# Kernel tuning notes

Hardware: AMD Instinct MI355X
Metric: run time of the kernel (lower is better)

## Reference

```python
import jax, jax.numpy as jnp
import numpy as np
from jax import lax

NUM_CLS = 80
N_INST = 100  # instances per image (static stand-in for NMS-selected boxes)
PARAM_DIM = 169  # (8+2)*8 + 8*8 + 8 + 8 + 8 + 1
MIC = 8  # mask_inner_channels


def conv2d(x, w, b=None, padding='SAME'):
    y = lax.conv_general_dilated(x, w, (1, 1), padding,
                                 dimension_numbers=('NCHW', 'OIHW', 'NCHW'))
    if b is not None:
        y = y + b[None, :, None, None]
    return y


def group_norm(x, g, b, groups, eps=1e-5):
    N, C, H, W = x.shape
    xr = x.reshape(N, groups, C // groups, H, W)
    mu = xr.mean(axis=(2, 3, 4), keepdims=True)
    var = xr.var(axis=(2, 3, 4), keepdims=True)
    xr = (xr - mu) * lax.rsqrt(var + eps)
    return xr.reshape(N, C, H, W) * g[None, :, None, None] + b[None, :, None, None]


def resize_bilinear_ac(x, oh, ow):
    # bilinear, align_corners=True (matches F.interpolate(..., align_corners=True))
    N, C, H, W = x.shape
    ys = jnp.linspace(0.0, H - 1.0, oh)
    xs = jnp.linspace(0.0, W - 1.0, ow)
    y0 = jnp.floor(ys).astype(jnp.int32); y1 = jnp.minimum(y0 + 1, H - 1); wy = (ys - y0).astype(x.dtype)
    x0 = jnp.floor(xs).astype(jnp.int32); x1 = jnp.minimum(x0 + 1, W - 1); wx = (xs - x0).astype(x.dtype)
    top = x[:, :, y0, :] * (1.0 - wy)[None, None, :, None] + x[:, :, y1, :] * wy[None, None, :, None]
    out = top[:, :, :, x0] * (1.0 - wx)[None, None, None, :] + top[:, :, :, x1] * wx[None, None, None, :]
    return out


def head_branch(f, head_w, head_gn_g, head_gn_b, head_out_w, head_out_b, scale):
    x = f
    for i in range(4):  # bones: conv3x3 (no bias) + GN(32) + ReLU
        x = jax.nn.relu(group_norm(conv2d(x, head_w[i]), head_gn_g[i], head_gn_b[i], 32))
    x = x * scale
    return conv2d(x, head_out_w, head_out_b)


def mask_branch(feats, ref_w, ref_gn_g, ref_gn_b, tow_w, tow_gn_g, tow_gn_b, out_w, out_gn_g, out_gn_b):
    x = None
    th, tw = feats[0].shape[2:]
    for i, f in enumerate(feats):
        xp = jax.nn.relu(group_norm(conv2d(f, ref_w[i]), ref_gn_g[i], ref_gn_b[i], 1))
        if i == 0:
            x = xp
        else:
            x = x + resize_bilinear_ac(xp, th, tw)
    for i in range(4):
        x = jax.nn.relu(group_norm(conv2d(x, tow_w[i]), tow_gn_g[i], tow_gn_b[i], 1))
    x = jax.nn.relu(group_norm(conv2d(x, out_w), out_gn_g, out_gn_b, 1))
    return x


def dynamic_conv(mask_feats, params):
    # mask_feats: [B, 8, h, w]; params: [B*N, 169] per-instance generated weights/biases
    B, C, h, w = mask_feats.shape
    n = params.shape[0]
    w1 = params[:, :80].reshape(n, MIC, C + 2)        # 1x1 conv 10->8
    w2 = params[:, 80:144].reshape(n, MIC, MIC)       # 1x1 conv 8->8
    w3 = params[:, 144:152].reshape(n, 1, MIC)        # 1x1 conv 8->1
    b1 = params[:, 152:160]
    b2 = params[:, 160:168]
    b3 = params[:, 168:169]
    # gather per-instance feature maps (img_ids = repeat of image index)
    x = jnp.repeat(mask_feats, n // B, axis=0)        # [n, 8, h, w]
    xr = jnp.linspace(-1.0, 1.0, w, dtype=mask_feats.dtype)
    yr = jnp.linspace(-1.0, 1.0, h, dtype=mask_feats.dtype)
    yy, xx = jnp.meshgrid(yr, xr, indexing='ij')
    coords = jnp.broadcast_to(jnp.stack([xx, yy], axis=0)[None], (n, 2, h, w))
    x = jnp.concatenate([x, coords], axis=1)          # [n, 10, h, w]
    x = jax.nn.relu(jnp.einsum('noc,nchw->nohw', w1, x) + b1[:, :, None, None])
    x = jax.nn.relu(jnp.einsum('noc,nchw->nohw', w2, x) + b2[:, :, None, None])
    x = jnp.einsum('noc,nchw->nohw', w3, x) + b3[:, :, None, None]
    return resize_bilinear_ac(x, 2 * h, 2 * w)        # [n, 1, 2h, 2w]


def condinst_forward(f3, f4, f5, f6, f7, head_w, head_gn_g, head_gn_b, head_out_w,
                     head_out_b, scales, ref_w, ref_gn_g, ref_gn_b, tow_w, tow_gn_g,
                     tow_gn_b, out_w, out_gn_g, out_gn_b):
    feats = [f3, f4, f5, f6, f7]
    preds = [head_branch(f, head_w, head_gn_g, head_gn_b, head_out_w, head_out_b, scales[i])
             for i, f in enumerate(feats)]
    mask_feats = mask_branch(feats[:3], ref_w, ref_gn_g, ref_gn_b,
                             tow_w, tow_gn_g, tow_gn_b, out_w, out_gn_g, out_gn_b)
    # controller params: take first N_INST P3 locations (static stand-in for NMS top-k)
    B = f3.shape[0]
    ctrl = preds[0][:, NUM_CLS + 5:, :, :].reshape(B, PARAM_DIM, -1)  # [B, 169, HW]
    params = jnp.transpose(ctrl[:, :, :N_INST], (0, 2, 1)).reshape(B * N_INST, PARAM_DIM)
    mask_logits = dynamic_conv(mask_feats, params)
    return (*preds, mask_feats, mask_logits)


def setup_inputs() -> dict:
    key = jax.random.key(0)
    ks = jax.random.split(key, 12)
    B = 2
    inp = {
        'f3': jax.random.normal(ks[0], (B, 256, 96, 160), jnp.float32),
        'f4': jax.random.normal(ks[1], (B, 256, 48, 80), jnp.float32),
        'f5': jax.random.normal(ks[2], (B, 256, 24, 40), jnp.float32),
        'f6': jax.random.normal(ks[3], (B, 256, 12, 20), jnp.float32),
        'f7': jax.random.normal(ks[4], (B, 256, 6, 10), jnp.float32),
        'head_w': 0.01 * jax.random.normal(ks[5], (4, 256, 256, 3, 3), jnp.float32),
        'head_gn_g': jnp.ones((4, 256), jnp.float32),
        'head_gn_b': jnp.zeros((4, 256), jnp.float32),
        'head_out_w': 0.01 * jax.random.normal(ks[6], (254, 256, 3, 3), jnp.float32),
        'head_out_b': jnp.zeros((254,), jnp.float32).at[:NUM_CLS].set(-np.log((1 - 0.01) / 0.01)),
        'scales': jnp.ones((5,), jnp.float32),
        'ref_w': 0.01 * jax.random.normal(ks[7], (3, 128, 256, 3, 3), jnp.float32),
        'ref_gn_g': jnp.ones((3, 128), jnp.float32),
        'ref_gn_b': jnp.zeros((3, 128), jnp.float32),
        'tow_w': 0.01 * jax.random.normal(ks[8], (4, 128, 128, 3, 3), jnp.float32),
        'tow_gn_g': jnp.ones((4, 128), jnp.float32),
        'tow_gn_b': jnp.zeros((4, 128), jnp.float32),
        'out_w': 0.01 * jax.random.normal(ks[9], (8, 128, 1, 1), jnp.float32),
        'out_gn_g': jnp.ones((8,), jnp.float32),
        'out_gn_b': jnp.zeros((8,), jnp.float32),
    }
    return inp


def reference(f3, f4, f5, f6, f7, head_w, head_gn_g, head_gn_b, head_out_w, head_out_b,
              scales, ref_w, ref_gn_g, ref_gn_b, tow_w, tow_gn_g, tow_gn_b, out_w,
              out_gn_g, out_gn_b):
    return condinst_forward(f3, f4, f5, f6, f7, head_w, head_gn_g, head_gn_b,
                            head_out_w, head_out_b, scales, ref_w, ref_gn_g, ref_gn_b,
                            tow_w, tow_gn_g, tow_gn_b, out_w, out_gn_g, out_gn_b)
```

## Files before the change

kernel.cpp:

```cpp
#include <hip/hip_runtime.h>
#include <hip/hip_bf16.h>

typedef __hip_bfloat16 bf16;
typedef short v8s __attribute__((ext_vector_type(8)));
typedef float v4f __attribute__((ext_vector_type(4)));

__device__ __forceinline__ float cvt(bf16 v) { return __bfloat162float(v); }

__device__ __forceinline__ float ldg_any(const void* p, size_t i, bool bf) {
    return bf ? cvt(((const bf16*)p)[i]) : ((const float*)p)[i];
}
__device__ __forceinline__ void stg_any(void* p, size_t i, float v, bool bf) {
    if (bf) ((bf16*)p)[i] = __float2bfloat16(v);
    else    ((float*)p)[i] = v;
}
__device__ __forceinline__ bool bfmode(int mode, const int* flags) {
    return mode == 2 ? (flags[0] != 0) : (mode != 0);
}
__device__ __forceinline__ unsigned short f2b(float f) {
    bf16 h = __float2bfloat16(f); return *(unsigned short*)&h;
}
__device__ __forceinline__ void b2f2(unsigned u, float& a, float& b) {
    a = __uint_as_float(u << 16);
    b = __uint_as_float(u & 0xffff0000u);
}

union U16x8 { uint4 u; unsigned short s[8]; };

#define BARLDS() asm volatile("s_waitcnt lgkmcnt(0)\n\ts_barrier" ::: "memory")

__global__ void detect_k(const unsigned int* __restrict__ x, int* __restrict__ flags)
{
    unsigned int u = x[threadIdx.x];
    int e = (u >> 23) & 0xFF;
    unsigned long long m = __ballot(e >= 200);
    if (threadIdx.x == 0) flags[0] = (m != 0ULL) ? 1 : 0;
}

__global__ void repack_off_k(const void* __restrict__ w, size_t w_off,
                             const int* __restrict__ flags, bf16* __restrict__ dst,
                             int Cout, int Cpad, int Cin, int total)
{
    const bool fw = flags[0] != 0;
    int i = blockIdx.x * 256 + threadIdx.x;
    if (i >= total) return;
    int ci = i % Cin; int r = i / Cin; int co = r % Cpad; int tap = r / Cpad;
    float v = 0.f;
    if (co < Cout) v = ldg_any(w, w_off + ((size_t)co * Cin + ci) * 9 + tap, fw);
    dst[i] = __float2bfloat16(v);
}

__global__ void padT_k(const void* __restrict__ src, const int* __restrict__ flags,
                       bf16* __restrict__ dst, int C, int H, int W, int Wq, int Hp,
                       int PIX, long total)
{
    const bool fb = flags[0] != 0;
    long v = (long)blockIdx.x * 256 + threadIdx.x;
    if (v >= total) return;
    const int C8 = C >> 3;
    int oct = (int)(v & (C8 - 1));
    long rest = v >> (C == 256 ? 5 : 4);
    int px = (int)(rest % Wq);
    long r2 = rest / Wq;
    int py = (int)(r2 % Hp);
    int n  = (int)(r2 / Hp);
    U16x8 o;
    if (py == 0 || py > H || px == 0 || px > W) {
        o.u = uint4{0, 0, 0, 0};
    } else {
        const int HW = H * W;
        size_t sb = ((size_t)n * C + oct * 8) * HW + (size_t)(py - 1) * W + (px - 1);
#pragma unroll
        for (int e = 0; e < 8; ++e) o.s[e] = f2b(ldg_any(src, sb + (size_t)e * HW, fb));
    }
    *(uint4*)(dst + v * 8) = o.u;
}

__global__ __launch_bounds__(256, 2) void conv3x3_mfma_k(
    const bf16* __restrict__ in,
    const bf16* __restrict__ wrep,
    const float* __restrict__ gstat, const void* __restrict__ gamma,
    const void* __restrict__ beta, size_t gb_off, int cpg, int Gn, float inv_pg,
    const void* __restrict__ bias, const void* __restrict__ scale, int sidx,
    void* __restrict__ out, int outm, size_t out_off, int out_C,
    const int* __restrict__ flags,
    int Cin, int H, int W, int Wq, int PIX, int Cout, int Cpad, int co_blocks)
{
    const bool fw   = flags[0] != 0;
    const bool fout = bfmode(outm, flags);

    const int t    = threadIdx.x;
    const int lane = t & 63;
    const int wv   = t >> 6;
    const int c    = lane & 15;
    const int quad = lane >> 4;
    const int wr   = wv >> 1;
    const int wc   = wv & 1;
    const int x0   = blockIdx.x * 32;
    const int y0   = blockIdx.y * 4;
    const int n    = blockIdx.z / co_blocks;
    const int cb   = blockIdx.z % co_blocks;

    __shared__ __align__(16) char s_arena[77312];
    float* s_scale = (float*)(s_arena + 75264);
    float* s_shift = (float*)(s_arena + 76288);

    const bool donorm = (gstat != nullptr);

    v4f acc[4][4];
#pragma unroll
    for (int i = 0; i < 4; ++i)
#pragma unroll
        for (int j = 0; j < 4; ++j) acc[i][j] = v4f{0.f, 0.f, 0.f, 0.f};

    const bf16* inb = in + (size_t)n * PIX * Cin;

    int goff[4], loff[4], okm[4], octv[4];
#pragma unroll
    for (int it = 0; it < 4; ++it) {
        int flat = t + 256 * it;
        int pos = flat >> 2, oct = flat & 3;
        int r = (pos * 241) >> 13;
        int cc = pos - r * 34;
        int py = y0 + r, px = x0 + cc;
        bool valid = flat < 816;
        goff[it] = (py * Wq + px) * Cin + oct * 8;
        loff[it] = valid ? (pos * 64 + (((oct + (pos >> 1)) & 3) << 4)) : -1;
        okm[it]  = (py >= 1 && py <= H && px >= 1 && px <= W) ? 1 : 0;
        octv[it] = oct * 8;
    }

    uint4 L[4];
    uint4 wrg[6];

#define STAGE_LOAD(ci0_) { \
    _Pragma("unroll") for (int it = 0; it < 4; ++it) \
        if (loff[it] >= 0) L[it] = *(const uint4*)(inb + goff[it] + (ci0_)); }

#define STAGE_WRITE(ci0_, b_) { \
    char* db = s_arena + (b_) * 13056; \
    _Pragma("unroll") for (int it = 0; it < 4; ++it) { \
        if (loff[it] < 0) continue; \
        uint4 q = L[it]; \
        if (donorm) { \
            U16x8 u_; u_.u = q; U16x8 o_; \
            if (okm[it]) { \
                int cib = (ci0_) + octv[it]; \
                _Pragma("unroll") for (int e = 0; e < 8; ++e) { \
                    float v_ = __uint_as_float((unsigned)u_.s[e] << 16); \
                    v_ = fmaxf(fmaf(v_, s_scale[cib + e], s_shift[cib + e]), 0.f); \
                    o_.s[e] = f2b(v_); } \
            } else { o_.u = uint4{0, 0, 0, 0}; } \
            q = o_.u; } \
        *(uint4*)(db + loff[it]) = q; } }

#define WLOAD(ci0_, g_) { \
    _Pragma("unroll") for (int j = 0; j < 6; ++j) { \
        int f_ = t + 256 * j; int tapl_ = f_ >> 9; int rem_ = f_ & 511; \
        wrg[j] = *(const uint4*)(wrep + ((size_t)(3 * (g_) + tapl_) * Cpad \
                 + cb * 128 + (rem_ >> 2)) * (size_t)Cin + (ci0_) + (rem_ & 3) * 8); } }

#define WSTORE(b_) { \
    bf16* sw = (bf16*)(s_arena + 26112 + (b_) * 24576); \
    _Pragma("unroll") for (int j = 0; j < 6; ++j) { \
        int f_ = t + 256 * j; int tapl_ = f_ >> 9; int rem_ = f_ & 511; \
        int co_ = rem_ >> 2; int oc_ = (rem_ + co_ + (co_ >> 2)) & 3; \
        *(uint4*)(&sw[tapl_ * 4096 + co_ * 32 + oc_ * 8]) = wrg[j]; } }

#define MPHASE(ib_, wb_, g_) { \
    const char* sb_ = s_arena + (ib_) * 13056; \
    const bf16* wp_ = (const bf16*)(s_arena + 26112 + (wb_) * 24576); \
    _Pragma("unroll") for (int kx = 0; kx < 3; ++kx) { \
        v8s bfr[4]; \
        _Pragma("unroll") for (int nf = 0; nf < 4; ++nf) { \
            int pos = (2 * wr + (nf >> 1) + (g_)) * 34 + kx + c + (nf & 1) * 16; \
            bfr[nf] = *(const v8s*)(sb_ + pos * 64 + (((quad + (pos >> 1)) & 3) << 4)); } \
        _Pragma("unroll") for (int mf = 0; mf < 4; ++mf) { \
            int col_ = wc * 64 + mf * 16 + c; \
            int os_ = (quad + col_ + (col_ >> 2)) & 3; \
            v8s af = *(const v8s*)(wp_ + kx * 4096 + col_ * 32 + os_ * 8); \
            _Pragma("unroll") for (int nf = 0; nf < 4; ++nf) \
                acc[mf][nf] = __builtin_amdgcn_mfma_f32_16x16x32_bf16( \
                    af, bfr[nf], acc[mf][nf], 0, 0, 0); } } }

    STAGE_LOAD(0);
    WLOAD(0, 0);
    if (donorm) {
        for (int ch = t; ch < Cin; ch += 256) {
            int gl = n * Gn + ch / cpg;
            float mu  = gstat[2 * gl] * inv_pg;
            float var = fmaxf(gstat[2 * gl + 1] * inv_pg - mu * mu, 0.f);
            float iv  = rsqrtf(var + 1e-5f);
            float ga  = ldg_any(gamma, gb_off + ch, fw);
            float be  = ldg_any(beta,  gb_off + ch, fw);
            s_scale[ch] = iv * ga;
            s_shift[ch] = be - mu * iv * ga;
        }
    }
    BARLDS();
    STAGE_WRITE(0, 0);
    WSTORE(0);
    BARLDS();

    for (int ci0 = 0; ci0 < Cin; ci0 += 64) {
        const bool moreB = (ci0 + 64 < Cin);
        STAGE_LOAD(ci0 + 32);
        WLOAD(ci0, 1);
        MPHASE(0, 0, 0);
        WSTORE(1);
        BARLDS();
        WLOAD(ci0, 2);
        MPHASE(0, 1, 1);
        WSTORE(0);
        BARLDS();
        WLOAD(ci0 + 32, 0);
        MPHASE(0, 0, 2);
        STAGE_WRITE(ci0 + 32, 1);
        WSTORE(1);
        BARLDS();
        if (moreB) STAGE_LOAD(ci0 + 64);
        WLOAD(ci0 + 32, 1);
        MPHASE(1, 1, 0);
        WSTORE(0);
        BARLDS();
        WLOAD(ci0 + 32, 2);
        MPHASE(1, 0, 1);
        WSTORE(1);
        BARLDS();
        if (moreB) { WLOAD(ci0 + 64, 0); }
        MPHASE(1, 1, 2);
        if (moreB) { STAGE_WRITE(ci0 + 64, 0); WSTORE(0); }
        BARLDS();
    }
#undef MPHASE
#undef WSTORE
#undef WLOAD
#undef STAGE_WRITE
#undef STAGE_LOAD

    if (outm == 0) {
        char* tb = s_arena;
#pragma unroll
        for (int mf = 0; mf < 4; ++mf) {
            int s0 = wc * 8 + mf * 2 + (quad >> 1);
#pragma unroll
            for (int nf = 0; nf < 4; ++nf) {
                int lp = (2 * wr + (nf >> 1)) * 32 + (nf & 1) * 16 + c;
                uint2 o;
                o.x = f2b(acc[mf][nf][0]) | ((unsigned)f2b(acc[mf][nf][1]) << 16);
                o.y = f2b(acc[mf][nf][2]) | ((unsigned)f2b(acc[mf][nf][3]) << 16);
                *(uint2*)(tb + lp * 256 + ((s0 ^ (lp & 7)) << 4) + (quad & 1) * 8) = o;
            }
        }
        BARLDS();
        bf16* ob = (bf16*)out + (size_t)n * PIX * out_C + cb * 128;
        const int o8 = t & 15;
#pragma unroll
        for (int pass = 0; pass < 8; ++pass) {
            int lp = pass * 16 + (t >> 4);
            uint4 q = *(const uint4*)(tb + lp * 256 + ((o8 ^ (lp & 7)) << 4));
            int y = y0 + (lp >> 5);
            int x = x0 + (lp & 31);
            if (y < H && x < W)
                *(uint4*)(ob + ((size_t)(y + 1) * Wq + (x + 1)) * out_C + o8 * 8) = q;
        }
    } else {
        const float al = scale ? ldg_any(scale, sidx, fw) : 1.f;
        const int HW = H * W;
        const int ybase = y0 + 2 * wr;
#pragma unroll
        for (int mf = 0; mf < 4; ++mf) {
            int cobase = cb * 128 + wc * 64 + mf * 16 + quad * 4;
#pragma unroll
            for (int reg = 0; reg < 4; ++reg) {
                int co = cobase + reg;
                if (co >= Cout) continue;
                float bv = bias ? ldg_any(bias, co, fw) : 0.f;
                size_t obase = out_off + ((size_t)n * Cout + co) * HW;
#pragma unroll
                for (int nf = 0; nf < 4; ++nf) {
                    int y = ybase + (nf >> 1);
                    int x = x0 + (nf & 1) * 16 + c;
                    if (y < H && x < W)
                        stg_any(out, obase + (size_t)y * W + x,
                                fmaf(al, acc[mf][nf][reg], bv), fout);
                }
            }
        }
    }
}

__global__ __launch_bounds__(256) void gn_stats_nhwc(const bf16* __restrict__ x,
                                                     float* __restrict__ stats,
                                                     int C8, int cpg8, int Gn,
                                                     long nvec, int planeC)
{
    const int n = blockIdx.z;
    const bf16* xp = x + (size_t)n * planeC;
    const int t = threadIdx.x;
    const int oct = t & (C8 - 1);
    float s = 0.f, ss = 0.f;
    const long stride = 256L * gridDim.x;
    for (long v = (long)blockIdx.x * 256 + t; v < nvec; v += stride) {
        uint4 u = *(const uint4*)(xp + v * 8);
        float f0,f1,f2,f3,f4,f5,f6,f7;
        b2f2(u.x, f0, f1); b2f2(u.y, f2, f3); b2f2(u.z, f4, f5); b2f2(u.w, f6, f7);
        s += ((f0+f1)+(f2+f3)) + ((f4+f5)+(f6+f7));
        ss = fmaf(f0,f0,ss); ss = fmaf(f1,f1,ss); ss = fmaf(f2,f2,ss); ss = fmaf(f3,f3,ss);
        ss = fmaf(f4,f4,ss); ss = fmaf(f5,f5,ss); ss = fmaf(f6,f6,ss); ss = fmaf(f7,f7,ss);
    }
    for (int off = C8; off < 64; off <<= 1) {
        s  += __shfl_xor(s,  off, 64);
        ss += __shfl_xor(ss, off, 64);
    }
    __shared__ float red[4][32][2];
    const int wvi = t >> 6;
    if ((t & 63) < C8) { red[wvi][oct][0] = s; red[wvi][oct][1] = ss; }
    __syncthreads();
    if (t < C8) {
        s  = red[0][t][0] + red[1][t][0] + red[2][t][0] + red[3][t][0];
        ss = red[0][t][1] + red[1][t][1] + red[2][t][1] + red[3][t][1];
        for (int off = cpg8 >> 1; off >= 1; off >>= 1) {
            s  += __shfl_down(s,  off, 64);
            ss += __shfl_down(ss, off, 64);
        }
        if ((t & (cpg8 - 1)) == 0) {
            int gl = n * Gn + t / cpg8;
            atomicAdd(&stats[2 * gl],     s);
            atomicAdd(&stats[2 * gl + 1], ss);
        }
    }
}

__global__ void gn_apply_nhwc(bf16* __restrict__ x, const float* __restrict__ stats,
                              const void* __restrict__ gamma, const void* __restrict__ beta,
                              size_t gb_off, const int* __restrict__ flags,
                              int C, int cpg, int Gn, int H, int W, int Wq, int PIX,
                              float inv_len, long total)
{
    const bool fw = flags[0] != 0;
    long v = (long)blockIdx.x * 256 + threadIdx.x;
    if (v >= total) return;
    const int C8 = C >> 3;
    int oct = (int)(v & (C8 - 1));
    long rest = v / C8;
    int x2 = (int)(rest % W);
    long r2 = rest / W;
    int y = (int)(r2 % H);
    int n = (int)(r2 / H);
    int ch0 = oct * 8;
    int gl = n * Gn + ch0 / cpg;
    float mu  = stats[2 * gl] * inv_len;
    float var = fmaxf(stats[2 * gl + 1] * inv_len - mu * mu, 0.f);
    float iv  = rsqrtf(var + 1e-5f);
    size_t base = ((size_t)n * PIX + (size_t)(y + 1) * Wq + (x2 + 1)) * C + ch0;
    U16x8 u; u.u = *(const uint4*)(x + base);
    U16x8 o;
#pragma unroll
    for (int e = 0; e < 8; ++e) {
        float ga = ldg_any(gamma, gb_off + ch0 + e, fw);
        float be = ldg_any(beta,  gb_off + ch0 + e, fw);
        float f = __uint_as_float((unsigned)u.s[e] << 16);
        f = fmaxf(fmaf(f, iv * ga, be - mu * iv * ga), 0.f);
        o.s[e] = f2b(f);
    }
    *(uint4*)(x + base) = o.u;
}

__global__ void extract_params_k(const void* __restrict__ pred3, const int* __restrict__ flags,
                                 float* __restrict__ prm, int HW)
{
    const bool bf = flags[0] != 0;
    int tid = blockIdx.x * blockDim.x + threadIdx.x;
    if (tid >= 200 * 169) return;
    int p = tid / 169, c = tid - p * 169;
    int b = p / 100, i = p - b * 100;
    prm[tid] = ldg_any(pred3, ((size_t)b * 254 + 85 + c) * HW + i, bf);
}

__global__ void upsample_add_nhwc(const bf16* __restrict__ src, bf16* __restrict__ dst,
                                  int h, int w, int sWq, int sPIX,
                                  int OH, int OW, int dWq, int dPIX, long total)
{
    long i = (long)blockIdx.x * 256 + threadIdx.x;
    if (i >= total) return;
    const int C = 128, C8 = 16;
    int oct = (int)(i & (C8 - 1));
    long rest = i >> 4;
    int ox = (int)(rest % OW);
    long r = rest / OW;
    int oy = (int)(r % OH);
    int n  = (int)(r / OH);
    float sy = oy * ((h - 1.f) / (OH - 1.f));
    float sx = ox * ((w - 1.f) / (OW - 1.f));
    int y0 = (int)sy; int y1 = min(y0 + 1, h - 1); float wy = sy - y0;
    int x0 = (int)sx; int x1 = min(x0 + 1, w - 1); float wx = sx - x0;
    const bf16* sp = src + (size_t)n * sPIX * C + oct * 8;
    U16x8 q00, q01, q10, q11;
    q00.u = *(const uint4*)(sp + ((size_t)(y0 + 1) * sWq + (x0 + 1)) * C);
    q01.u = *(const uint4*)(sp + ((size_t)(y0 + 1) * sWq + (x1 + 1)) * C);
    q10.u = *(const uint4*)(sp + ((size_t)(y1 + 1) * sWq + (x0 + 1)) * C);
    q11.u = *(const uint4*)(sp + ((size_t)(y1 + 1) * sWq + (x1 + 1)) * C);
    bf16* dp = dst + ((size_t)n * dPIX + (size_t)(oy + 1) * dWq + (ox + 1)) * C + oct * 8;
    U16x8 d; d.u = *(const uint4*)dp;
    U16x8 o;
#pragma unroll
    for (int e = 0; e < 8; ++e) {
        float a00 = __uint_as_float((unsigned)q00.s[e] << 16);
        float a01 = __uint_as_float((unsigned)q01.s[e] << 16);
        float a10 = __uint_as_float((unsigned)q10.s[e] << 16);
        float a11 = __uint_as_float((unsigned)q11.s[e] << 16);
        float t0 = a00 * (1.f - wy) + a10 * wy;
        float t1 = a01 * (1.f - wy) + a11 * wy;
        float dv = __uint_as_float((unsigned)d.s[e] << 16);
        o.s[e] = f2b(dv + t0 * (1.f - wx) + t1 * wx);
    }
    *(uint4*)dp = o.u;
}

__global__ void resize_out_k(const float* __restrict__ src, void* __restrict__ dst,
                             size_t dst_off, const int* __restrict__ flags,
                             int h, int w, int OH, int OW, long total)
{
    const bool bf = flags[0] != 0;
    long i = (long)blockIdx.x * blockDim.x + threadIdx.x;
    if (i >= total) return;
    int ox = (int)(i % OW);
    long r = i / OW;
    int oy = (int)(r % OH);
    int nc = (int)(r / OH);
    float sy = oy * ((h - 1.f) / (OH - 1.f));
    float sx = ox * ((w - 1.f) / (OW - 1.f));
    int y0 = (int)sy; int y1 = min(y0 + 1, h - 1); float wy = sy - y0;
    int x0 = (int)sx; int x1 = min(x0 + 1, w - 1); float wx = sx - x0;
    const float* sp = src + (size_t)nc * h * w;
    float t0 = sp[y0 * w + x0] * (1.f - wy) + sp[y1 * w + x0] * wy;
    float t1 = sp[y0 * w + x1] * (1.f - wy) + sp[y1 * w + x1] * wy;
    stg_any(dst, dst_off + (size_t)i, t0 * (1.f - wx) + t1 * wx, bf);
}

__global__ void cast_out_k(const bf16* __restrict__ src, void* __restrict__ dst,
                           size_t dst_off, const int* __restrict__ flags, long n)
{
    const bool bf = flags[0] != 0;
    long i = (long)blockIdx.x * blockDim.x + threadIdx.x;
    if (i < n) stg_any(dst, dst_off + (size_t)i, cvt(src[i]), bf);
}

__global__ __launch_bounds__(256) void conv1x1_nhwc(const bf16* __restrict__ in,
                                                    const void* __restrict__ w,
                                                    const int* __restrict__ flags,
                                                    bf16* __restrict__ out,
                                                    int H, int W, int Wq, int PIX)
{
    const bool fw = flags[0] != 0;
    __shared__ float sw[8 * 128];
    for (int i = threadIdx.x; i < 1024; i += 256) sw[i] = ldg_any(w, i, fw);
    __syncthreads();
    const int HW = H * W;
    int idx = blockIdx.x * 256 + threadIdx.x;
    if (idx >= 2 * HW) return;
    int pix = idx % HW, n = idx / HW;
    int y = pix / W, x = pix - y * W;
    const bf16* ip = in + ((size_t)n * PIX + (size_t)(y + 1) * Wq + (x + 1)) * 128;
    float a[8];
#pragma unroll
    for (int o = 0; o < 8; ++o) a[o] = 0.f;
    for (int oc = 0; oc < 16; ++oc) {
        U16x8 q; q.u = *(const uint4*)(ip + oc * 8);
#pragma unroll
        for (int e = 0; e < 8; ++e) {
            float f = __uint_as_float((unsigned)q.s[e] << 16);
#pragma unroll
            for (int o = 0; o < 8; ++o) a[o] = fmaf(sw[o * 128 + oc * 8 + e], f, a[o]);
        }
    }
#pragma unroll
    for (int o = 0; o < 8; ++o)
        out[((size_t)n * 8 + o) * HW + pix] = __float2bfloat16(a[o]);
}

__global__ __launch_bounds__(256) void gn_stats_v(const bf16* __restrict__ x,
                                                  float* __restrict__ stats, int per_group)
{
    const int g = blockIdx.x;
    const uint4* xp = (const uint4*)(x + (size_t)g * per_group);
    const int nvec = per_group >> 3;
    float s = 0.f, ss = 0.f;
    const int stride = 256 * gridDim.y;
    for (int i = blockIdx.y * 256 + threadIdx.x; i < nvec; i += stride) {
        uint4 u = xp[i];
        float f0,f1,f2,f3,f4,f5,f6,f7;
        b2f2(u.x, f0, f1); b2f2(u.y, f2, f3); b2f2(u.z, f4, f5); b2f2(u.w, f6, f7);
        s += ((f0+f1)+(f2+f3)) + ((f4+f5)+(f6+f7));
        ss = fmaf(f0,f0,ss); ss = fmaf(f1,f1,ss); ss = fmaf(f2,f2,ss); ss = fmaf(f3,f3,ss);
        ss = fmaf(f4,f4,ss); ss = fmaf(f5,f5,ss); ss = fmaf(f6,f6,ss); ss = fmaf(f7,f7,ss);
    }
#pragma unroll
    for (int off = 32; off > 0; off >>= 1) {
        s  += __shfl_down(s,  off, 64);
        ss += __shfl_down(ss, off, 64);
    }
    __shared__ float sh[8];
    const int wv = threadIdx.x >> 6;
    if ((threadIdx.x & 63) == 0) { sh[wv * 2] = s; sh[wv * 2 + 1] = ss; }
    __syncthreads();
    if (threadIdx.x == 0) {
        s  = sh[0] + sh[2] + sh[4] + sh[6];
        ss = sh[1] + sh[3] + sh[5] + sh[7];
        atomicAdd(&stats[2 * g],     s);
        atomicAdd(&stats[2 * g + 1], ss);
    }
}

__global__ void gn_apply_v(bf16* __restrict__ x, const float* __restrict__ stats,
                           const void* __restrict__ gamma, const void* __restrict__ beta,
                           size_t gb_off, const int* __restrict__ flags,
                           int HW, int C, int per_group, float inv_len, long nvec)
{
    const bool fw = flags[0] != 0;
    long v = (long)blockIdx.x * blockDim.x + threadIdx.x;
    if (v >= nvec) return;
    long i0 = v * 8;
    int gl = (int)(i0 / per_group);
    float mu  = stats[2 * gl] * inv_len;
    float var = fmaxf(stats[2 * gl + 1] * inv_len - mu * mu, 0.f);
    float iv  = rsqrtf(var + 1e-5f);
    int cc = (int)((i0 / HW) % C);
    float ga = ldg_any(gamma, gb_off + cc, fw);
    float be = ldg_any(beta,  gb_off + cc, fw);
    float sc = iv * ga, sf = be - mu * iv * ga;
    uint4 u = *(const uint4*)(x + i0);
    float f[8];
    b2f2(u.x, f[0], f[1]); b2f2(u.y, f[2], f[3]);
    b2f2(u.z, f[4], f[5]); b2f2(u.w, f[6], f[7]);
#pragma unroll
    for (int j = 0; j < 8; ++j) f[j] = fmaxf(fmaf(f[j], sc, sf), 0.f);
    uint4 o;
    o.x = f2b(f[0]) | ((unsigned)f2b(f[1]) << 16);
    o.y = f2b(f[2]) | ((unsigned)f2b(f[3]) << 16);
    o.z = f2b(f[4]) | ((unsigned)f2b(f[5]) << 16);
    o.w = f2b(f[6]) | ((unsigned)f2b(f[7]) << 16);
    *(uint4*)(x + i0) = o;
}

__global__ __launch_bounds__(256) void dyn_conv_k(const bf16* __restrict__ mf,
                                                  const float* __restrict__ prm,
                                                  float* __restrict__ out, int H, int W)
{
    const int inst = blockIdx.y;
    __shared__ float p[169];
    if (threadIdx.x < 169) p[threadIdx.x] = prm[inst * 169 + threadIdx.x];
    __syncthreads();
    const int HW = H * W;
    const int pix = blockIdx.x * 256 + threadIdx.x;
    if (pix >= HW) return;
    const int b = inst / 100;
    float xin[10];
#pragma unroll
    for (int c = 0; c < 8; ++c) xin[c] = cvt(mf[((size_t)(b * 8 + c)) * HW + pix]);
    int yy = pix / W, xx = pix - yy * W;
    xin[8] = -1.f + 2.f * xx / (W - 1);
    xin[9] = -1.f + 2.f * yy / (H - 1);
    float h1[8];
#pragma unroll
    for (int o = 0; o < 8; ++o) {
        float s = p[152 + o];
#pragma unroll
        for (int c = 0; c < 10; ++c) s = fmaf(p[o * 10 + c], xin[c], s);
        h1[o] = fmaxf(s, 0.f);
    }
    float h2[8];
#pragma unroll
    for (int o = 0; o < 8; ++o) {
        float s = p[160 + o];
#pragma unroll
        for (int c = 0; c < 8; ++c) s = fmaf(p[80 + o * 8 + c], h1[c], s);
        h2[o] = fmaxf(s, 0.f);
    }
    float s = p[168];
#pragma unroll
    for (int c = 0; c < 8; ++c) s = fmaf(p[144 + c], h2[c], s);
    out[(size_t)inst * HW + pix] = s;
}

struct Norm { const float* st; const void* g; const void* b; size_t off; int cpg; int Gn; float inv; };
struct Geo  { int H, W, Wq, Hp, PIX; };

static inline Geo mkgeo(int H, int W) {
    int xb = (W + 31) / 32, yb = (H + 3) / 4;
    Geo g; g.H = H; g.W = W; g.Wq = (xb - 1) * 32 + 34; g.Hp = (yb - 1) * 4 + 6;
    g.PIX = g.Hp * g.Wq;
    return g;
}

static inline void mconv(const bf16* in, const bf16* wrep, const Norm* nm,
                         const void* bias, const void* scale, int sidx,
                         void* out, int outm, size_t out_off, int out_C,
                         const int* flags, int N, int Cin, Geo g, int Cout, hipStream_t s)
{
    int cob = (Cout + 127) / 128, Cpad = cob * 128;
    dim3 gr((g.W + 31) / 32, (g.H + 3) / 4, N * cob);
    conv3x3_mfma_k<<<gr, 256, 0, s>>>(
        in, wrep,
        nm ? nm->st : nullptr, nm ? nm->g : nullptr, nm ? nm->b : nullptr,
        nm ? nm->off : 0, nm ? nm->cpg : 1, nm ? nm->Gn : 1, nm ? nm->inv : 1.f,
        bias, scale, sidx, out, outm, out_off, out_C,
        flags, Cin, g.H, g.W, g.Wq, g.PIX, Cout, Cpad, cob);
}

static inline void run_padT(const void* src, const int* flags, bf16* dst,
                            int N, int C, Geo g, hipStream_t s)
{
    long total = (long)N * g.PIX * (C >> 3);
    padT_k<<<(int)((total + 255) / 256), 256, 0, s>>>(src, flags, dst, C, g.H, g.W,
                                                      g.Wq, g.Hp, g.PIX, total);
}

static inline void run_stats_nhwc(const bf16* x, float* st, int N, int C, int cpg, int Gn,
                                  Geo g, hipStream_t s)
{
    int C8 = C >> 3;
    long nvec = (long)g.PIX * C8;
    int chunks = (int)((nvec + 16383) / 16384);
    if (chunks > 32) chunks = 32; if (chunks < 1) chunks = 1;
    gn_stats_nhwc<<<dim3(chunks, 1, N), 256, 0, s>>>(x, st, C8, cpg >> 3, Gn,
                                                     nvec, g.PIX * C);
}

static inline void run_apply_nhwc(bf16* x, const float* st, const void* gm, const void* bt,
                                  size_t off, const int* flags, int N, int C, int cpg, int Gn,
                                  Geo g, hipStream_t s)
{
    long total = (long)N * g.H * g.W * (C >> 3);
    gn_apply_nhwc<<<(int)((total + 255) / 256), 256, 0, s>>>(
        x, st, gm, bt, off, flags, C, cpg, Gn, g.H, g.W, g.Wq, g.PIX,
        1.f / ((float)cpg * g.H * g.W), total);
}

extern "C" void kernel_launch(void* const* d_in, const int* in_sizes, int n_in,
                              void* d_out, int out_size, void* d_ws, size_t ws_size,
                              hipStream_t stream)
{
    const void* f[5] = {d_in[0], d_in[1], d_in[2], d_in[3], d_in[4]};
    static const int Hs[5] = {96, 48, 24, 12, 6};
    static const int Wd[5] = {160, 80, 40, 20, 10};
    const void* head_w     = d_in[5];
    const void* head_gn_g  = d_in[6];
    const void* head_gn_b  = d_in[7];
    const void* head_out_w = d_in[8];
    const void* head_out_b = d_in[9];
    const void* scales     = d_in[10];
    const void* ref_w      = d_in[11];
    const void* ref_gn_g   = d_in[12];
    const void* ref_gn_b   = d_in[13];
    const void* tow_w      = d_in[14];
    const void* tow_gn_g   = d_in[15];
    const void* tow_gn_b   = d_in[16];
    const void* out_w      = d_in[17];
    const void* out_gn_g   = d_in[18];
    const void* out_gn_b   = d_in[19];

    Geo G[5];
    for (int l = 0; l < 5; ++l) G[l] = mkgeo(Hs[l], Wd[l]);

    size_t po[5]; size_t off = 0;
    for (int l = 0; l < 5; ++l) { po[l] = off; off += (size_t)2 * 254 * Hs[l] * Wd[l]; }
    size_t mf_off = off; off += 245760;
    size_t ml_off = off;

    const size_t ACAP = (size_t)2 * 256 * G[0].PIX;
    bf16*  A     = (bf16*)d_ws;
    bf16*  B     = A + ACAP;
    bf16*  B2    = B + ACAP;
    bf16*  mfeat = B2 + 1254400;
    float* prm   = (float*)(mfeat + 245760);
    float* stats = prm + 33800;
    int*   flags = (int*)(stats + 4096);
    bf16*  wrep  = (bf16*)(flags + 16);
    float* dyn   = (float*)A;

    bf16* wrepH  = wrep;
    bf16* wrepHO = wrep + 4 * 589824;
    bf16* wrepR  = wrep;
    bf16* wrepT  = wrep + 3 * 294912;

    hipMemsetAsync(stats, 0, 4096 * sizeof(float), stream);
    detect_k<<<1, 64, 0, stream>>>((const unsigned int*)d_in[0], flags);

    float* sp = stats;

    for (int l = 0; l < 4; ++l) {
        int total = 9 * 256 * 256;
        repack_off_k<<<(total + 255) / 256, 256, 0, stream>>>(
            head_w, (size_t)l * 589824, flags, wrepH + (size_t)l * 589824, 256, 256, 256, total);
    }
    {
        int total = 9 * 256 * 256;
        repack_off_k<<<(total + 255) / 256, 256, 0, stream>>>(
            head_out_w, 0, flags, wrepHO, 254, 256, 256, total);
    }

    for (int lvl = 0; lvl < 5; ++lvl) {
        Geo g = G[lvl];
        int HW = g.H * g.W;
        float inv_pg = 1.f / (8 * HW);
        run_padT(f[lvl], flags, B, 2, 256, g, stream);
        hipMemsetAsync(A, 0, (size_t)2 * 256 * g.PIX * sizeof(bf16), stream);
        mconv(B, wrepH, nullptr, nullptr, nullptr, 0, A, 0, 0, 256,
              flags, 2, 256, g, 256, stream);
        float* s_prev = sp; sp += 128;
        run_stats_nhwc(A, s_prev, 2, 256, 8, 32, g, stream);
        bf16* a = A; bf16* bb = B;
        for (int l = 1; l < 4; ++l) {
            Norm nm{s_prev, head_gn_g, head_gn_b, (size_t)(l - 1) * 256, 8, 32, inv_pg};
            mconv(a, wrepH + (size_t)l * 589824, &nm, nullptr, nullptr, 0,
                  bb, 0, 0, 256, flags, 2, 256, g, 256, stream);
            s_prev = sp; sp += 128;
            run_stats_nhwc(bb, s_prev, 2, 256, 8, 32, g, stream);
            bf16* tmp = a; a = bb; bb = tmp;
        }
        Norm nm{s_prev, head_gn_g, head_gn_b, (size_t)3 * 256, 8, 32, inv_pg};
        mconv(a, wrepHO, &nm, head_out_b, scales, lvl, d_out, 2, po[lvl], 0,
              flags, 2, 256, g, 254, stream);
        if (lvl == 0)
            extract_params_k<<<(200 * 169 + 255) / 256, 256, 0, stream>>>(d_out, flags, prm, HW);
    }

    for (int i = 0; i < 3; ++i) {
        int total = 9 * 128 * 256;
        repack_off_k<<<(total + 255) / 256, 256, 0, stream>>>(
            ref_w, (size_t)i * 294912, flags, wrepR + (size_t)i * 294912, 128, 128, 256, total);
    }
    for (int l = 0; l < 4; ++l) {
        int total = 9 * 128 * 128;
        repack_off_k<<<(total + 255) / 256, 256, 0, stream>>>(
            tow_w, (size_t)l * 147456, flags, wrepT + (size_t)l * 147456, 128, 128, 128, total);
    }

    {
        Geo g0 = G[0];
        const int HW = 96 * 160;

        run_padT(f[0], flags, B, 2, 256, g0, stream);
        hipMemsetAsync(A, 0, (size_t)2 * 128 * g0.PIX * sizeof(bf16), stream);
        mconv(B, wrepR, nullptr, nullptr, nullptr, 0, A, 0, 0, 128,
              flags, 2, 256, g0, 128, stream);
        float* s0 = sp; sp += 4;
        run_stats_nhwc(A, s0, 2, 128, 128, 1, g0, stream);
        run_apply_nhwc(A, s0, ref_gn_g, ref_gn_b, 0, flags, 2, 128, 128, 1, g0, stream);

        for (int i = 1; i < 3; ++i) {
            Geo gi = G[i];
            run_padT(f[i], flags, B, 2, 256, gi, stream);
            hipMemsetAsync(B2, 0, (size_t)2 * 128 * gi.PIX * sizeof(bf16), stream);
            mconv(B, wrepR + (size_t)i * 294912, nullptr, nullptr, nullptr, 0,
                  B2, 0, 0, 128, flags, 2, 256, gi, 128, stream);
            float* si = sp; sp += 4;
            run_stats_nhwc(B2, si, 2, 128, 128, 1, gi, stream);
            run_apply_nhwc(B2, si, ref_gn_g, ref_gn_b, (size_t)i * 128, flags,
                           2, 128, 128, 1, gi, stream);
            long tot = (long)2 * 96 * 160 * 16;
            upsample_add_nhwc<<<(int)((tot + 255) / 256), 256, 0, stream>>>(
                B2, A, gi.H, gi.W, gi.Wq, gi.PIX, 96, 160, g0.Wq, g0.PIX, tot);
        }

        float inv_pg = 1.f / (128 * HW);
        hipMemsetAsync(B, 0, (size_t)2 * 128 * g0.PIX * sizeof(bf16), stream);
        mconv(A, wrepT, nullptr, nullptr, nullptr, 0, B, 0, 0, 128,
              flags, 2, 128, g0, 128, stream);
        float* sT = sp; sp += 4;
        run_stats_nhwc(B, sT, 2, 128, 128, 1, g0, stream);
        bf16* a = B; bf16* bb = A;
        for (int l = 1; l < 4; ++l) {
            Norm nm{sT, tow_gn_g, tow_gn_b, (size_t)(l - 1) * 128, 128, 1, inv_pg};
            mconv(a, wrepT + (size_t)l * 147456, &nm, nullptr, nullptr, 0,
                  bb, 0, 0, 128, flags, 2, 128, g0, 128, stream);
            sT = sp; sp += 4;
            run_stats_nhwc(bb, sT, 2, 128, 128, 1, g0, stream);
            bf16* tmp = a; a = bb; bb = tmp;
        }
        run_apply_nhwc(a, sT, tow_gn_g, tow_gn_b, (size_t)3 * 128, flags, 2, 128, 128, 1, g0, stream);
        conv1x1_nhwc<<<(2 * HW + 255) / 256, 256, 0, stream>>>(
            a, out_w, flags, mfeat, 96, 160, g0.Wq, g0.PIX);
        float* sM = sp; sp += 4;
        {
            int chunks = (8 * HW) / 8192; if (chunks < 1) chunks = 1;
            gn_stats_v<<<dim3(2, chunks), 256, 0, stream>>>(mfeat, sM, 8 * HW);
            long nvec = ((long)2 * 8 * HW) >> 3;
            gn_apply_v<<<(int)((nvec + 255) / 256), 256, 0, stream>>>(
                mfeat, sM, out_gn_g, out_gn_b, 0, flags, HW, 8, 8 * HW, 1.f / (8 * HW), nvec);
        }
        cast_out_k<<<(2 * 8 * HW + 255) / 256, 256, 0, stream>>>(
            mfeat, d_out, mf_off, flags, (long)2 * 8 * HW);
        dyn_conv_k<<<dim3((HW + 255) / 256, 200), 256, 0, stream>>>(mfeat, prm, dyn, 96, 160);
        long nt = (long)200 * 192 * 320;
        resize_out_k<<<(int)((nt + 255) / 256), 256, 0, stream>>>(
            dyn, d_out, ml_off, flags, 96, 160, 192, 320, nt);
    }
}
```

Measured before the change: 2.435 ms.

## Fuse GroupNorm statistics reduction into conv3x3 MFMA epilogue

Computes per-channel sums and sums of squares from the conv accumulators in the MFMA kernel epilogue. These are reduced across lanes, waves and groups, then atomically added into the stats buffer. This removes the separate gn_stats_nhwc pass that re-read every conv output from global memory. The cost is an extra LDS barrier and shuffle work per block, plus many more atomics. The stats are also taken from fp32 accumulators rather than the bf16-rounded outputs, which slightly changes the numerics.

```diff
diff --git a/kernel.cpp b/kernel.cpp
--- a/kernel.cpp
+++ b/kernel.cpp
@@ -84,7 +84,8 @@
     const void* __restrict__ bias, const void* __restrict__ scale, int sidx,
     void* __restrict__ out, int outm, size_t out_off, int out_C,
     const int* __restrict__ flags,
-    int Cin, int H, int W, int Wq, int PIX, int Cout, int Cpad, int co_blocks)
+    int Cin, int H, int W, int Wq, int PIX, int Cout, int Cpad, int co_blocks,
+    float* __restrict__ ostat, int ocpg8, int oGn)
 {
     const bool fw   = flags[0] != 0;
     const bool fout = bfmode(outm, flags);
@@ -102,6 +103,7 @@
     const int cb   = blockIdx.z % co_blocks;
 
     __shared__ __align__(16) char s_arena[77312];
+    __shared__ float s_srd[4][8][2];
     float* s_scale = (float*)(s_arena + 75264);
     float* s_shift = (float*)(s_arena + 76288);
 
@@ -238,6 +240,56 @@
 #undef STAGE_WRITE
 #undef STAGE_LOAD
 
+    if (ostat) {
+        float ps[4], pq[4];
+#pragma unroll
+        for (int mf = 0; mf < 4; ++mf) { ps[mf] = 0.f; pq[mf] = 0.f; }
+#pragma unroll
+        for (int nf = 0; nf < 4; ++nf) {
+            int y = y0 + 2 * wr + (nf >> 1);
+            int x = x0 + (nf & 1) * 16 + c;
+            bool ok = (y < H) && (x < W);
+#pragma unroll
+            for (int mf = 0; mf < 4; ++mf)
+#pragma unroll
+                for (int reg = 0; reg < 4; ++reg) {
+                    float v = ok ? acc[mf][nf][reg] : 0.f;
+                    ps[mf] += v;
+                    pq[mf] = fmaf(v, v, pq[mf]);
+                }
+        }
+#pragma unroll
+        for (int off = 1; off <= 16; off <<= 1)
+#pragma unroll
+            for (int mf = 0; mf < 4; ++mf) {
+                ps[mf] += __shfl_xor(ps[mf], off, 64);
+                pq[mf] += __shfl_xor(pq[mf], off, 64);
+            }
+        if (c == 0 && ((quad & 1) == 0)) {
+            int qh = quad >> 1;
+#pragma unroll
+            for (int mf = 0; mf < 4; ++mf) {
+                s_srd[wv][mf * 2 + qh][0] = ps[mf];
+                s_srd[wv][mf * 2 + qh][1] = pq[mf];
+            }
+        }
+        BARLDS();
+        if (t < 16) {
+            int wcl = t >> 3, idx = t & 7;
+            float s  = s_srd[wcl][idx][0] + s_srd[wcl + 2][idx][0];
+            float ss = s_srd[wcl][idx][1] + s_srd[wcl + 2][idx][1];
+            for (int off = ocpg8 >> 1; off >= 1; off >>= 1) {
+                s  += __shfl_down(s,  off, 64);
+                ss += __shfl_down(ss, off, 64);
+            }
+            if ((t & (ocpg8 - 1)) == 0) {
+                int gl = n * oGn + (cb * 16 + t) / ocpg8;
+                atomicAdd(&ostat[2 * gl],     s);
+                atomicAdd(&ostat[2 * gl + 1], ss);
+            }
+        }
+    }
+
     if (outm == 0) {
         char* tb = s_arena;
 #pragma unroll
@@ -286,48 +338,6 @@
                                 fmaf(al, acc[mf][nf][reg], bv), fout);
                 }
             }
-        }
-    }
-}
-
-__global__ __launch_bounds__(256) void gn_stats_nhwc(const bf16* __restrict__ x,
-                                                     float* __restrict__ stats,
-                                                     int C8, int cpg8, int Gn,
-                                                     long nvec, int planeC)
-{
-    const int n = blockIdx.z;
-    const bf16* xp = x + (size_t)n * planeC;
-    const int t = threadIdx.x;
-    const int oct = t & (C8 - 1);
-    float s = 0.f, ss = 0.f;
-    const long stride = 256L * gridDim.x;
-    for (long v = (long)blockIdx.x * 256 + t; v < nvec; v += stride) {
-        uint4 u = *(const uint4*)(xp + v * 8);
-        float f0,f1,f2,f3,f4,f5,f6,f7;
-        b2f2(u.x, f0, f1); b2f2(u.y, f2, f3); b2f2(u.z, f4, f5); b2f2(u.w, f6, f7);
-        s += ((f0+f1)+(f2+f3)) + ((f4+f5)+(f6+f7));
-        ss = fmaf(f0,f0,ss); ss = fmaf(f1,f1,ss); ss = fmaf(f2,f2,ss); ss = fmaf(f3,f3,ss);
-        ss = fmaf(f4,f4,ss); ss = fmaf(f5,f5,ss); ss = fmaf(f6,f6,ss); ss = fmaf(f7,f7,ss);
-    }
-    for (int off = C8; off < 64; off <<= 1) {
-        s  += __shfl_xor(s,  off, 64);
-        ss += __shfl_xor(ss, off, 64);
-    }
-    __shared__ float red[4][32][2];
-    const int wvi = t >> 6;
-    if ((t & 63) < C8) { red[wvi][oct][0] = s; red[wvi][oct][1] = ss; }
-    __syncthreads();
-    if (t < C8) {
-        s  = red[0][t][0] + red[1][t][0] + red[2][t][0] + red[3][t][0];
-        ss = red[0][t][1] + red[1][t][1] + red[2][t][1] + red[3][t][1];
-        for (int off = cpg8 >> 1; off >= 1; off >>= 1) {
-            s  += __shfl_down(s,  off, 64);
-            ss += __shfl_down(ss, off, 64);
-        }
-        if ((t & (cpg8 - 1)) == 0) {
-            int gl = n * Gn + t / cpg8;
-            atomicAdd(&stats[2 * gl],     s);
-            atomicAdd(&stats[2 * gl + 1], ss);
         }
     }
 }
@@ -597,7 +607,8 @@
 static inline void mconv(const bf16* in, const bf16* wrep, const Norm* nm,
                          const void* bias, const void* scale, int sidx,
                          void* out, int outm, size_t out_off, int out_C,
-                         const int* flags, int N, int Cin, Geo g, int Cout, hipStream_t s)
+                         const int* flags, int N, int Cin, Geo g, int Cout,
+                         float* ostat, int ocpg8, int oGn, hipStream_t s)
 {
     int cob = (Cout + 127) / 128, Cpad = cob * 128;
     dim3 gr((g.W + 31) / 32, (g.H + 3) / 4, N * cob);
@@ -606,7 +617,8 @@
         nm ? nm->st : nullptr, nm ? nm->g : nullptr, nm ? nm->b : nullptr,
         nm ? nm->off : 0, nm ? nm->cpg : 1, nm ? nm->Gn : 1, nm ? nm->inv : 1.f,
         bias, scale, sidx, out, outm, out_off, out_C,
-        flags, Cin, g.H, g.W, g.Wq, g.PIX, Cout, Cpad, cob);
+        flags, Cin, g.H, g.W, g.Wq, g.PIX, Cout, Cpad, cob,
+        ostat, ocpg8, oGn);
 }
 
 static inline void run_padT(const void* src, const int* flags, bf16* dst,
@@ -615,17 +627,6 @@
     long total = (long)N * g.PIX * (C >> 3);
     padT_k<<<(int)((total + 255) / 256), 256, 0, s>>>(src, flags, dst, C, g.H, g.W,
                                                       g.Wq, g.Hp, g.PIX, total);
-}
-
-static inline void run_stats_nhwc(const bf16* x, float* st, int N, int C, int cpg, int Gn,
-                                  Geo g, hipStream_t s)
-{
-    int C8 = C >> 3;
-    long nvec = (long)g.PIX * C8;
-    int chunks = (int)((nvec + 16383) / 16384);
-    if (chunks > 32) chunks = 32; if (chunks < 1) chunks = 1;
-    gn_stats_nhwc<<<dim3(chunks, 1, N), 256, 0, s>>>(x, st, C8, cpg >> 3, Gn,
-                                                     nvec, g.PIX * C);
 }
 
 static inline void run_apply_nhwc(bf16* x, const float* st, const void* gm, const void* bt,
@@ -707,22 +708,21 @@
         float inv_pg = 1.f / (8 * HW);
         run_padT(f[lvl], flags, B, 2, 256, g, stream);
         hipMemsetAsync(A, 0, (size_t)2 * 256 * g.PIX * sizeof(bf16), stream);
+        float* s_prev = sp; sp += 128;
         mconv(B, wrepH, nullptr, nullptr, nullptr, 0, A, 0, 0, 256,
-              flags, 2, 256, g, 256, stream);
-        float* s_prev = sp; sp += 128;
-        run_stats_nhwc(A, s_prev, 2, 256, 8, 32, g, stream);
+              flags, 2, 256, g, 256, s_prev, 1, 32, stream);
         bf16* a = A; bf16* bb = B;
         for (int l = 1; l < 4; ++l) {
             Norm nm{s_prev, head_gn_g, head_gn_b, (size_t)(l - 1) * 256, 8, 32, inv_pg};
+            float* s_cur = sp; sp += 128;
             mconv(a, wrepH + (size_t)l * 589824, &nm, nullptr, nullptr, 0,
-                  bb, 0, 0, 256, flags, 2, 256, g, 256, stream);
-            s_prev = sp; sp += 128;
-            run_stats_nhwc(bb, s_prev, 2, 256, 8, 32, g, stream);
+                  bb, 0, 0, 256, flags, 2, 256, g, 256, s_cur, 1, 32, stream);
+            s_prev = s_cur;
             bf16* tmp = a; a = bb; bb = tmp;
         }
         Norm nm{s_prev, head_gn_g, head_gn_b, (size_t)3 * 256, 8, 32, inv_pg};
         mconv(a, wrepHO, &nm, head_out_b, scales, lvl, d_out, 2, po[lvl], 0,
-              flags, 2, 256, g, 254, stream);
+              flags, 2, 256, g, 254, nullptr, 1, 1, stream);
         if (lvl == 0)
             extract_params_k<<<(200 * 169 + 255) / 256, 256, 0, stream>>>(d_out, flags, prm, HW);
     }
@@ -744,20 +744,18 @@
 
         run_padT(f[0], flags, B, 2, 256, g0, stream);
         hipMemsetAsync(A, 0, (size_t)2 * 128 * g0.PIX * sizeof(bf16), stream);
+        float* s0 = sp; sp += 4;
         mconv(B, wrepR, nullptr, nullptr, nullptr, 0, A, 0, 0, 128,
-              flags, 2, 256, g0, 128, stream);
-        float* s0 = sp; sp += 4;
-        run_stats_nhwc(A, s0, 2, 128, 128, 1, g0, stream);
+              flags, 2, 256, g0, 128, s0, 16, 1, stream);
         run_apply_nhwc(A, s0, ref_gn_g, ref_gn_b, 0, flags, 2, 128, 128, 1, g0, stream);
 
         for (int i = 1; i < 3; ++i) {
             Geo gi = G[i];
             run_padT(f[i], flags, B, 2, 256, gi, stream);
             hipMemsetAsync(B2, 0, (size_t)2 * 128 * gi.PIX * sizeof(bf16), stream);
+            float* si = sp; sp += 4;
             mconv(B, wrepR + (size_t)i * 294912, nullptr, nullptr, nullptr, 0,
-                  B2, 0, 0, 128, flags, 2, 256, gi, 128, stream);
-            float* si = sp; sp += 4;
-            run_stats_nhwc(B2, si, 2, 128, 128, 1, gi, stream);
+                  B2, 0, 0, 128, flags, 2, 256, gi, 128, si, 16, 1, stream);
             run_apply_nhwc(B2, si, ref_gn_g, ref_gn_b, (size_t)i * 128, flags,
                            2, 128, 128, 1, gi, stream);
             long tot = (long)2 * 96 * 160 * 16;
@@ -767,17 +765,16 @@
 
         float inv_pg = 1.f / (128 * HW);
         hipMemsetAsync(B, 0, (size_t)2 * 128 * g0.PIX * sizeof(bf16), stream);
+        float* sT = sp; sp += 4;
         mconv(A, wrepT, nullptr, nullptr, nullptr, 0, B, 0, 0, 128,
-              flags, 2, 128, g0, 128, stream);
-        float* sT = sp; sp += 4;
-        run_stats_nhwc(B, sT, 2, 128, 128, 1, g0, stream);
+              flags, 2, 128, g0, 128, sT, 16, 1, stream);
         bf16* a = B; bf16* bb = A;
         for (int l = 1; l < 4; ++l) {
             Norm nm{sT, tow_gn_g, tow_gn_b, (size_t)(l - 1) * 128, 128, 1, inv_pg};
+            float* sN = sp; sp += 4;
             mconv(a, wrepT + (size_t)l * 147456, &nm, nullptr, nullptr, 0,
-                  bb, 0, 0, 128, flags, 2, 128, g0, 128, stream);
-            sT = sp; sp += 4;
-            run_stats_nhwc(bb, sT, 2, 128, 128, 1, g0, stream);
+                  bb, 0, 0, 128, flags, 2, 128, g0, 128, sN, 16, 1, stream);
+            sT = sN;
             bf16* tmp = a; a = bb; bb = tmp;
         }
         run_apply_nhwc(a, sT, tow_gn_g, tow_gn_b, (size_t)3 * 128, flags, 2, 128, 128, 1, g0, stream);
```

Result: faster. 2.076 ms (-14.8%).
